# Kernel tuning notes

Measured on AMD Instinct MI355X. Metric: run time of the kernel, lower is better.

The kernel has to match this reference:

```python
import math
import jax, jax.numpy as jnp
import numpy as np

B, S, M, D, H, FF = 2, 2048, 64, 1024, 16, 4096
HD = D // H


def setup_inputs() -> dict:
    key = jax.random.key(0)
    ks = jax.random.split(key, 16)
    w = lambda k, shape: jax.random.normal(k, shape, dtype=jnp.float32) * 0.02
    # RoPE angles: theta_i = pos / 10000^(2i/head_dim)
    inv_freq = 1.0 / (10000.0 ** (jnp.arange(0, HD, 2, dtype=jnp.float32) / HD))
    ang = jnp.arange(S, dtype=jnp.float32)[:, None] * inv_freq[None, :]  # (S, HD//2)
    return {
        "tgt": jax.random.normal(ks[0], (B, S, D), dtype=jnp.float32),
        "memory": jax.random.normal(ks[1], (B, M, D), dtype=jnp.float32),
        "rope_cos": jnp.cos(ang),
        "rope_sin": jnp.sin(ang),
        "W_qkv": w(ks[2], (D, 3 * D)), "b_qkv": jnp.zeros((3 * D,), jnp.float32),
        "W_o": w(ks[3], (D, D)), "b_o": jnp.zeros((D,), jnp.float32),
        "Wq_c": w(ks[4], (D, D)), "bq_c": jnp.zeros((D,), jnp.float32),
        "Wk_c": w(ks[5], (D, D)), "bk_c": jnp.zeros((D,), jnp.float32),
        "Wv_c": w(ks[6], (D, D)), "bv_c": jnp.zeros((D,), jnp.float32),
        "W_co": w(ks[7], (D, D)), "b_co": jnp.zeros((D,), jnp.float32),
        "W1": w(ks[8], (D, FF)), "b1": jnp.zeros((FF,), jnp.float32),
        "W2": w(ks[9], (FF, D)), "b2": jnp.zeros((D,), jnp.float32),
        "g1": jnp.ones((D,), jnp.float32), "be1": jnp.zeros((D,), jnp.float32),
        "g2": jnp.ones((D,), jnp.float32), "be2": jnp.zeros((D,), jnp.float32),
        "g3": jnp.ones((D,), jnp.float32), "be3": jnp.zeros((D,), jnp.float32),
    }


def _layer_norm(x, g, b, eps=1e-5):
    mu = jnp.mean(x, axis=-1, keepdims=True)
    var = jnp.mean(jnp.square(x - mu), axis=-1, keepdims=True)
    return (x - mu) * jax.lax.rsqrt(var + eps) * g + b


def _apply_rope(x, cos, sin):
    # x: (B, H, S, HD); cos/sin: (S, HD//2). Pairs (even, odd) rotated as complex.
    xe, xo = x[..., 0::2], x[..., 1::2]
    c = cos[None, None]
    s = sin[None, None]
    re = xe * c - xo * s
    im = xe * s + xo * c
    return jnp.stack([re, im], axis=-1).reshape(x.shape)


def reference(tgt, memory, rope_cos, rope_sin, W_qkv, b_qkv, W_o, b_o,
              Wq_c, bq_c, Wk_c, bk_c, Wv_c, bv_c, W_co, b_co,
              W1, b1, W2, b2, g1, be1, g2, be2, g3, be3):
    b, s, d = tgt.shape
    scale = 1.0 / math.sqrt(HD)

    # --- RoPE self-attention (causal) ---
    x = _layer_norm(tgt, g1, be1)
    qkv = (x @ W_qkv + b_qkv).reshape(b, s, 3, H, HD)
    qkv = jnp.transpose(qkv, (2, 0, 3, 1, 4))  # (3, b, H, s, HD)
    q, k, v = qkv[0], qkv[1], qkv[2]
    q = _apply_rope(q, rope_cos[:s], rope_sin[:s])
    k = _apply_rope(k, rope_cos[:s], rope_sin[:s])
    attn = jnp.einsum('bhqd,bhkd->bhqk', q, k) * scale
    causal = jnp.tril(jnp.ones((s, s), dtype=bool))
    attn = jnp.where(causal[None, None], attn, -1e9)
    attn = jax.nn.softmax(attn, axis=-1)
    sa = jnp.einsum('bhqk,bhkd->bhqd', attn, v)
    sa = jnp.transpose(sa, (0, 2, 1, 3)).reshape(b, s, d)
    tgt = tgt + (sa @ W_o + b_o)

    # --- cross-attention to memory (no positional encoding) ---
    x = _layer_norm(tgt, g2, be2)
    m = memory.shape[1]
    qc = (x @ Wq_c + bq_c).reshape(b, s, H, HD).transpose(0, 2, 1, 3)
    kc = (memory @ Wk_c + bk_c).reshape(b, m, H, HD).transpose(0, 2, 1, 3)
    vc = (memory @ Wv_c + bv_c).reshape(b, m, H, HD).transpose(0, 2, 1, 3)
    ca = jax.nn.softmax(jnp.einsum('bhqd,bhkd->bhqk', qc, kc) * scale, axis=-1)
    co = jnp.einsum('bhqk,bhkd->bhqd', ca, vc)
    co = jnp.transpose(co, (0, 2, 1, 3)).reshape(b, s, d)
    tgt = tgt + (co @ W_co + b_co)

    # --- FFN (exact GELU, dropout disabled = eval) ---
    x = _layer_norm(tgt, g3, be3)
    ffn = jax.nn.gelu(x @ W1 + b1, approximate=False) @ W2 + b2
    return tgt + ffn
```

## Files before the change

kernel.cpp:

```cpp
#include <hip/hip_runtime.h>

typedef unsigned short u16;
typedef short bf16x8 __attribute__((ext_vector_type(8)));
typedef float f32x4 __attribute__((ext_vector_type(4)));

#define HN 16
#define SD 64
#define SEQ 2048
#define DM 1024
#define QSC 0.18033688f

__device__ __forceinline__ float bf2f(u16 h) {
  return __uint_as_float(((unsigned int)h) << 16);
}
__device__ __forceinline__ u16 f2bf(float f) {
  unsigned int x = __float_as_uint(f);
  x += 0x7fffu + ((x >> 16) & 1u);
  return (u16)(x >> 16);
}
__device__ __forceinline__ float geluf(float x) {
  return 0.5f * x * (1.0f + erff(x * 0.70710678118654752f));
}
__device__ __forceinline__ void load_lds16(const u16* g, u16* l) {
  __builtin_amdgcn_global_load_lds(
      (const __attribute__((address_space(1))) void*)g,
      (__attribute__((address_space(3))) void*)l, 16, 0, 0);
}

__device__ __forceinline__ void trans_tile(const float* __restrict__ in,
                                           u16* __restrict__ out, int K, int N,
                                           int tx, int ty, int tid,
                                           u16 (*T)[72]) {
  const int n0 = tx * 64, k0 = ty * 64;
#pragma unroll
  for (int it = 0; it < 2; ++it) {
    const int t = it * 256 + tid, r = t >> 3, c = (t & 7) * 8;
    const float* src = &in[(size_t)(k0 + r) * N + n0 + c];
    float4 d0 = *(const float4*)src;
    float4 d1 = *(const float4*)(src + 4);
    T[r][c + 0] = f2bf(d0.x);
    T[r][c + 1] = f2bf(d0.y);
    T[r][c + 2] = f2bf(d0.z);
    T[r][c + 3] = f2bf(d0.w);
    T[r][c + 4] = f2bf(d1.x);
    T[r][c + 5] = f2bf(d1.y);
    T[r][c + 6] = f2bf(d1.z);
    T[r][c + 7] = f2bf(d1.w);
  }
  __syncthreads();
#pragma unroll
  for (int it = 0; it < 2; ++it) {
    const int t = it * 256 + tid, r = t >> 3, c = (t & 7) * 8;
    uint4 d;
    u16* p = (u16*)&d;
#pragma unroll
    for (int j = 0; j < 8; ++j) p[j] = T[c + j][r];
    *(uint4*)&out[(size_t)(n0 + r) * K + k0 + c] = d;
  }
}

__global__ __launch_bounds__(256) void prep1(
    const float* __restrict__ Wqkv, const float* __restrict__ Wo,
    const float* __restrict__ Wqc, const float* __restrict__ Wkc,
    const float* __restrict__ Wvc, const float* __restrict__ Wco,
    u16* __restrict__ Tqkv, u16* __restrict__ To, u16* __restrict__ Tqc,
    u16* __restrict__ Tkc, u16* __restrict__ Tvc, u16* __restrict__ Tco,
    const float* __restrict__ mem, u16* __restrict__ memb) {
  __shared__ u16 T[64][72];
  const int t = blockIdx.x, tid = threadIdx.x;
  if (t < 768) {
    trans_tile(Wqkv, Tqkv, 1024, 3072, t % 48, t / 48, tid, T);
    return;
  }
  if (t < 2048) {
    const int u = t - 768, m = u >> 8, sub = u & 255;
    const float* in;
    u16* out;
    if (m == 0) { in = Wo; out = To; }
    else if (m == 1) { in = Wqc; out = Tqc; }
    else if (m == 2) { in = Wkc; out = Tkc; }
    else if (m == 3) { in = Wvc; out = Tvc; }
    else { in = Wco; out = Tco; }
    trans_tile(in, out, 1024, 1024, sub & 15, sub >> 4, tid, T);
    return;
  }
  const int i = ((t - 2048) * 256 + tid) * 4;
  float4 d = *(const float4*)&mem[i];
  uint2 o;
  u16* po = (u16*)&o;
  po[0] = f2bf(d.x);
  po[1] = f2bf(d.y);
  po[2] = f2bf(d.z);
  po[3] = f2bf(d.w);
  *(uint2*)&memb[i] = o;
}

__global__ __launch_bounds__(256) void prep2(const float* __restrict__ W1,
                                             const float* __restrict__ W2,
                                             u16* __restrict__ T1,
                                             u16* __restrict__ T2) {
  __shared__ u16 T[64][72];
  const int t = blockIdx.x, tid = threadIdx.x;
  if (t < 1024) {
    trans_tile(W1, T1, 1024, 4096, t & 63, t >> 6, tid, T);
  } else {
    const int u = t - 1024;
    trans_tile(W2, T2, 4096, 1024, u & 15, u >> 4, tid, T);
  }
}

__global__ __launch_bounds__(256) void ln_kernel(
    const float* __restrict__ x, const float* __restrict__ g,
    const float* __restrict__ be, u16* __restrict__ y) {
  const int row = blockIdx.x, tid = threadIdx.x;
  const float* xr = x + (size_t)row * DM;
  float4 d = *(const float4*)&xr[tid * 4];
  float v[4] = {d.x, d.y, d.z, d.w};
  float s1 = 0.f, s2 = 0.f;
#pragma unroll
  for (int j = 0; j < 4; ++j) {
    s1 += v[j];
    s2 += v[j] * v[j];
  }
#pragma unroll
  for (int dd = 1; dd < 64; dd <<= 1) {
    s1 += __shfl_xor(s1, dd, 64);
    s2 += __shfl_xor(s2, dd, 64);
  }
  __shared__ float p1[4], p2[4];
  const int lane = tid & 63, wv = tid >> 6;
  if (lane == 0) {
    p1[wv] = s1;
    p2[wv] = s2;
  }
  __syncthreads();
  s1 = p1[0] + p1[1] + p1[2] + p1[3];
  s2 = p2[0] + p2[1] + p2[2] + p2[3];
  const float mu = s1 * (1.f / DM);
  const float rs = rsqrtf(fmaxf(s2 * (1.f / DM) - mu * mu, 0.f) + 1e-5f);
  float4 gg = *(const float4*)&g[tid * 4];
  float4 bb = *(const float4*)&be[tid * 4];
  const float gv[4] = {gg.x, gg.y, gg.z, gg.w};
  const float bv[4] = {bb.x, bb.y, bb.z, bb.w};
  uint2 o;
  u16* po = (u16*)&o;
#pragma unroll
  for (int j = 0; j < 4; ++j) po[j] = f2bf((v[j] - mu) * rs * gv[j] + bv[j]);
  *(uint2*)&y[(size_t)row * DM + tid * 4] = o;
}

template <int EPI, int TM>
__global__ __launch_bounds__(256) void gemm_bt(
    const u16* __restrict__ A, const u16* __restrict__ Bt,
    const float* __restrict__ bias, const float* __restrict__ resid,
    void* __restrict__ C0, u16* __restrict__ C1, u16* __restrict__ C2, int M,
    int N, int K, int rpbl, float sc, const float* __restrict__ rcos,
    const float* __restrict__ rsin) {
  constexpr int MI = TM / 32;
  __shared__ __align__(16) u16 As[TM][64];
  __shared__ __align__(16) u16 Bs[128][64];
  const int tid = threadIdx.x;
  const int lane = tid & 63, wv = tid >> 6;
  const int l16 = lane & 15, quad = lane >> 4;

  if (EPI == 6 && blockIdx.z) {
    Bt = (const u16*)C1;
    bias = resid;
  }

  int bx = blockIdx.x, by = blockIdx.y;
  const int gx = gridDim.x, gy = gridDim.y;
  if ((gy & 7) == 0) {
    const int f = by * gx + bx;
    const int c = f & 7, j = f >> 3;
    const int jm = j / gx;
    by = c * (gy >> 3) + jm;
    bx = j - jm * gx;
  }
  const int m0 = by * TM, n0 = bx * 128;
  const int wm = (wv >> 1) * (TM / 2), wn = (wv & 1) * 64;

  const int srow = lane >> 3;
  const int sblk = (lane & 7) ^ srow;
  const u16* ag[MI];
  const u16* bg[4];
  u16* la[MI];
  u16* lb[4];
#pragma unroll
  for (int i = 0; i < MI; ++i) {
    const int r0 = i * 32 + wv * 8;
    ag[i] = A + (size_t)(m0 + r0 + srow) * K + sblk * 8;
    la[i] = &As[r0][0] + lane * 8;
  }
#pragma unroll
  for (int i = 0; i < 4; ++i) {
    const int r0 = i * 32 + wv * 8;
    bg[i] = Bt + (size_t)(n0 + r0 + srow) * K + sblk * 8;
    lb[i] = &Bs[r0][0] + lane * 8;
  }

  f32x4 acc[MI][4] = {};

  for (int k0 = 0; k0 < K; k0 += 64) {
    __syncthreads();
#pragma unroll
    for (int i = 0; i < MI; ++i) load_lds16(ag[i] + k0, la[i]);
#pragma unroll
    for (int i = 0; i < 4; ++i) load_lds16(bg[i] + k0, lb[i]);
    __syncthreads();
#pragma unroll
    for (int kk = 0; kk < 2; ++kk) {
      bf16x8 af[MI], bfr[4];
#pragma unroll
      for (int mi = 0; mi < MI; ++mi) {
        const int row = wm + mi * 16 + l16;
        const int blk = (kk * 4 + quad) ^ (row & 7);
        af[mi] = *(const bf16x8*)&As[row][blk * 8];
      }
#pragma unroll
      for (int ni = 0; ni < 4; ++ni) {
        const int row = wn + ni * 16 + l16;
        const int blk = (kk * 4 + quad) ^ (row & 7);
        bfr[ni] = *(const bf16x8*)&Bs[row][blk * 8];
      }
#pragma unroll
      for (int mi = 0; mi < MI; ++mi)
#pragma unroll
        for (int ni = 0; ni < 4; ++ni)
          acc[mi][ni] = __builtin_amdgcn_mfma_f32_16x16x32_bf16(
              af[mi], bfr[ni], acc[mi][ni], 0, 0, 0);
    }
  }

  const int SL = 1 << rpbl;
#pragma unroll
  for (int mi = 0; mi < MI; ++mi) {
#pragma unroll
    for (int ni = 0; ni < 4; ++ni) {
#pragma unroll
      for (int r = 0; r < 4; ++r) {
        const int row = m0 + wm + mi * 16 + quad * 4 + r;
        const int col = n0 + wn + ni * 16 + l16;
        float vv = acc[mi][ni][r] + bias[col];
        if (EPI == 1) {
          vv += resid[(size_t)row * N + col];
          ((float*)C0)[(size_t)row * N + col] = vv;
        } else if (EPI == 2) {
          ((u16*)C0)[(size_t)row * N + col] = f2bf(geluf(vv));
        } else if (EPI == 3) {
          const float partner = __shfl_xor(vv, 1);
          const int which = col >> 10;
          const int nn = col & 1023;
          const int h = nn >> 6, hd = nn & 63;
          const int b = row >> rpbl;
          const int s = row & (SL - 1);
          if (which == 2) {
            C2[(((size_t)b * HN + h) * SD + hd) * SL + s] = f2bf(vv);
          } else {
            const int p = hd >> 1;
            const float cv = rcos[s * 32 + p];
            const float sv2 = rsin[s * 32 + p];
            float o = (hd & 1) ? (partner * sv2 + vv * cv)
                               : (vv * cv - partner * sv2);
            if (which == 0) o *= QSC;
            u16* dst = (which == 0) ? (u16*)C0 : C1;
            dst[(((size_t)b * HN + h) * SL + s) * SD + hd] = f2bf(o);
          }
        } else if (EPI == 4) {
          vv *= sc;
          const int h = col >> 6, hd = col & 63;
          const int b = row >> rpbl;
          const int s = row & (SL - 1);
          ((u16*)C0)[(((size_t)b * HN + h) * SL + s) * SD + hd] = f2bf(vv);
        } else if (EPI == 5) {
          const int h = col >> 6, hd = col & 63;
          const int b = row >> rpbl;
          const int s = row & (SL - 1);
          ((u16*)C0)[(((size_t)b * HN + h) * SD + hd) * SL + s] = f2bf(vv);
        } else if (EPI == 6) {
          const int h = col >> 6, hd = col & 63;
          const int b = row >> rpbl;
          const int s = row & (SL - 1);
          if (blockIdx.z == 0)
            ((u16*)C0)[(((size_t)b * HN + h) * SL + s) * SD + hd] = f2bf(vv);
          else
            C2[(((size_t)b * HN + h) * SD + hd) * SL + s] = f2bf(vv);
        } else {
          ((u16*)C0)[(size_t)row * N + col] = f2bf(vv);
        }
      }
    }
  }
}

template <int EPI>
__global__ __launch_bounds__(512, 2) void gemm8p(
    const u16* __restrict__ A, const u16* __restrict__ Bt,
    const float* __restrict__ bias, void* __restrict__ C0,
    u16* __restrict__ C1, u16* __restrict__ C2, int M, int N, int K, int rpbl,
    const float* __restrict__ rcos, const float* __restrict__ rsin) {
  __shared__ __align__(16) u16 L[4][2][8192];
  const int tid = threadIdx.x;
  const int lane = tid & 63, wv = tid >> 6;
  const int l16 = lane & 15, quad = lane >> 4;
  const int bx = blockIdx.x, by = blockIdx.y;
  const int m0 = by * 256, n0 = bx * 256;
  const int wm = (wv >> 2) * 128, wn = (wv & 3) * 64;
  const int nk = K >> 6;

  const u16* Ag = A + (size_t)m0 * K;
  const u16* Bg = Bt + (size_t)n0 * K;

  auto stage = [&](int mat, int h, int st) {
    const int tt = st < nk ? st : nk - 1;
    const int k0 = tt << 6;
    u16* dst = &L[mat * 2 + h][st & 1][0];
    const u16* src = mat ? Bg : Ag;
#pragma unroll
    for (int j = 0; j < 2; ++j) {
      const int li = wv * 2 + j;
      const int p = li * 8 + (lane >> 3);
      const int b = lane & 7;
      const int g = b ^ (p & 7);
      const int row = 2 * p + (g >> 2);
      load_lds16(src + (size_t)row * K + k0 + h * 32 + (g & 3) * 8,
                 dst + li * 512 + lane * 8);
    }
  };

  f32x4 acc[8][4] = {};
  bf16x8 bfr[4];

#define PHASE(CB, KK, MH, RB, SM, SH, ST, VM)                                \
  {                                                                          \
    const u16* Ar = &L[KK][CB][0];                                           \
    const u16* Br = &L[2 + KK][CB][0];                                       \
    bf16x8 af[4];                                                            \
    _Pragma("unroll") for (int mi = 0; mi < 4; ++mi) {                       \
      const int R = wm + MH * 64 + mi * 16 + l16;                            \
      const int p = R >> 1, g = (R & 1) * 4 + quad, b = g ^ (p & 7);         \
      af[mi] = *(const bf16x8*)&Ar[p * 64 + b * 8];                          \
    }                                                                        \
    if (RB) {                                                                \
      _Pragma("unroll") for (int ni = 0; ni < 4; ++ni) {                     \
        const int R = wn + ni * 16 + l16;                                    \
        const int p = R >> 1, g = (R & 1) * 4 + quad, b = g ^ (p & 7);       \
        bfr[ni] = *(const bf16x8*)&Br[p * 64 + b * 8];                       \
      }                                                                      \
    }                                                                        \
    stage(SM, SH, ST);                                                       \
    __builtin_amdgcn_s_barrier();                                            \
    asm volatile("s_waitcnt lgkmcnt(0)" ::: "memory");                       \
    __builtin_amdgcn_s_setprio(1);                                           \
    _Pragma("unroll") for (int mi = 0; mi < 4; ++mi)                         \
        _Pragma("unroll") for (int ni = 0; ni < 4; ++ni) acc[MH * 4 + mi]    \
            [ni] = __builtin_amdgcn_mfma_f32_16x16x32_bf16(                  \
                af[mi], bfr[ni], acc[MH * 4 + mi][ni], 0, 0, 0);             \
    __builtin_amdgcn_s_setprio(0);                                           \
    if (VM) asm volatile("s_waitcnt vmcnt(8)" ::: "memory");                 \
    __builtin_amdgcn_s_barrier();                                            \
  }

  stage(0, 0, 0);
  stage(1, 0, 0);
  stage(0, 1, 0);
  stage(1, 1, 0);
  stage(0, 0, 1);
  stage(1, 0, 1);
  asm volatile("s_waitcnt vmcnt(8)" ::: "memory");
  __builtin_amdgcn_s_barrier();

  for (int t = 0; t < nk; ++t) {
    const int cb = t & 1;
    PHASE(cb, 0, 0, true, 0, 1, t + 1, false)
    PHASE(cb, 0, 1, false, 1, 1, t + 1, true)
    PHASE(cb, 1, 0, true, 0, 0, t + 2, false)
    PHASE(cb, 1, 1, false, 1, 0, t + 2, true)
  }
#undef PHASE

  const int SL = 1 << rpbl;
#pragma unroll
  for (int mi = 0; mi < 8; ++mi) {
#pragma unroll
    for (int ni = 0; ni < 4; ++ni) {
#pragma unroll
      for (int r = 0; r < 4; ++r) {
        const int row = m0 + wm + mi * 16 + quad * 4 + r;
        const int col = n0 + wn + ni * 16 + l16;
        float vv = acc[mi][ni][r] + bias[col];
        if (EPI == 2) {
          ((u16*)C0)[(size_t)row * N + col] = f2bf(geluf(vv));
        } else if (EPI == 3) {
          const float partner = __shfl_xor(vv, 1);
          const int which = col >> 10;
          const int nn = col & 1023;
          const int h = nn >> 6, hd = nn & 63;
          const int b = row >> rpbl;
          const int s = row & (SL - 1);
          if (which == 2) {
            C2[(((size_t)b * HN + h) * SD + hd) * SL + s] = f2bf(vv);
          } else {
            const int p = hd >> 1;
            const float cv = rcos[s * 32 + p];
            const float sv2 = rsin[s * 32 + p];
            float o = (hd & 1) ? (partner * sv2 + vv * cv)
                               : (vv * cv - partner * sv2);
            if (which == 0) o *= QSC;
            u16* dst = (which == 0) ? (u16*)C0 : C1;
            dst[(((size_t)b * HN + h) * SL + s) * SD + hd] = f2bf(o);
          }
        } else {
          ((u16*)C0)[(size_t)row * N + col] = f2bf(vv);
        }
      }
    }
  }
}

template <int CAUSAL>
__global__ __launch_bounds__(512, 4) void attn_kernel(
    const u16* __restrict__ q, const u16* __restrict__ k,
    const u16* __restrict__ vt, u16* __restrict__ out, int kv_len) {
  __shared__ u16 Qs[128][72], Ks[64][72], VTs[64][72];
  __shared__ u16 Ps[128][68];
  const int tid = threadIdx.x;
  const int lane = tid & 63, wv = tid >> 6;
  const int t2 = wv >> 2, w4 = wv & 3;
  const int l16 = lane & 15, quad = lane >> 4;
  const int bx = blockIdx.x, bh = blockIdx.y;
  const int qtA = bx;
  const int qtB = CAUSAL ? (31 - bx) : (bx + 16);
  const int qt = t2 ? qtB : qtA;
  const u16* qb = q + (size_t)bh * SEQ * SD;
  const u16* kb = k + (size_t)bh * kv_len * SD;
  const u16* vtb = vt + (size_t)bh * SD * kv_len;

#pragma unroll
  for (int it = 0; it < 2; ++it) {
    const int t = it * 512 + tid, r = t >> 3, c = (t & 7) * 8;
    const int qrow = (r < 64) ? (qtA * 64 + r) : (qtB * 64 + (r - 64));
    *(uint4*)&Qs[r][c] = *(const uint4*)&qb[(size_t)qrow * SD + c];
  }

  f32x4 o_acc[4] = {};
  float l_i[4] = {};

  const int ktiles = CAUSAL ? (qtB + 1) : ((kv_len + 63) >> 6);
  const int sr = tid >> 3, sc8 = (tid & 7) * 8;

  for (int kt = 0; kt < ktiles; ++kt) {
    const uint4 kd = *(const uint4*)&kb[((size_t)kt * 64 + sr) * SD + sc8];
    const uint4 vd = *(const uint4*)&vtb[(size_t)sr * kv_len + kt * 64 + sc8];
    __syncthreads();
    *(uint4*)&Ks[sr][sc8] = kd;
    *(uint4*)&VTs[sr][sc8] = vd;
    __syncthreads();

    if (kt <= qt) {
      const int roff = t2 * 64 + w4 * 16;
      f32x4 s_acc[4] = {};
#pragma unroll
      for (int kk = 0; kk < 64; kk += 32) {
        const bf16x8 aq = *(const bf16x8*)&Qs[roff + l16][kk + quad * 8];
#pragma unroll
        for (int ni = 0; ni < 4; ++ni) {
          const bf16x8 bk = *(const bf16x8*)&Ks[ni * 16 + l16][kk + quad * 8];
          s_acc[ni] = __builtin_amdgcn_mfma_f32_16x16x32_bf16(aq, bk, s_acc[ni],
                                                              0, 0, 0);
        }
      }
      float rsum[4] = {0.f, 0.f, 0.f, 0.f};
      const bool dg = CAUSAL && (kt == qt);
#pragma unroll
      for (int ni = 0; ni < 4; ++ni)
#pragma unroll
        for (int r = 0; r < 4; ++r) {
          float sv = s_acc[ni][r];
          if (dg && (ni * 16 + l16 > w4 * 16 + quad * 4 + r)) sv = -1e9f;
          const float pe = __builtin_amdgcn_exp2f(sv);
          rsum[r] += pe;
          Ps[wv * 16 + quad * 4 + r][ni * 16 + l16] =
              (u16)(__float_as_uint(pe) >> 16);
        }
#pragma unroll
      for (int r = 0; r < 4; ++r) {
#pragma unroll
        for (int dd = 1; dd < 16; dd <<= 1)
          rsum[r] += __shfl_xor(rsum[r], dd, 64);
        l_i[r] += rsum[r];
      }
#pragma unroll
      for (int kk = 0; kk < 64; kk += 32) {
        const bf16x8 ap = *(const bf16x8*)&Ps[wv * 16 + l16][kk + quad * 8];
#pragma unroll
        for (int ni = 0; ni < 4; ++ni) {
          const bf16x8 bv = *(const bf16x8*)&VTs[ni * 16 + l16][kk + quad * 8];
          o_acc[ni] = __builtin_amdgcn_mfma_f32_16x16x32_bf16(ap, bv, o_acc[ni],
                                                              0, 0, 0);
        }
      }
    }
  }

  const int b = bh >> 4, h = bh & 15;
#pragma unroll
  for (int r = 0; r < 4; ++r) {
    const float inv = 1.f / l_i[r];
    const int s = qt * 64 + w4 * 16 + quad * 4 + r;
#pragma unroll
    for (int ni = 0; ni < 4; ++ni)
      out[((size_t)b * SEQ + s) * DM + h * SD + ni * 16 + l16] =
          f2bf(o_acc[ni][r] * inv);
  }
}

extern "C" void kernel_launch(void* const* d_in, const int* in_sizes, int n_in,
                              void* d_out, int out_size, void* d_ws,
                              size_t ws_size, hipStream_t stream) {
  (void)in_sizes;
  (void)n_in;
  (void)out_size;
  (void)ws_size;
  const float* tgt = (const float*)d_in[0];
  const float* mem = (const float*)d_in[1];
  const float* rc = (const float*)d_in[2];
  const float* rsn = (const float*)d_in[3];
  const float* W_qkv = (const float*)d_in[4];
  const float* b_qkv = (const float*)d_in[5];
  const float* W_o = (const float*)d_in[6];
  const float* b_o = (const float*)d_in[7];
  const float* Wq_c = (const float*)d_in[8];
  const float* bq_c = (const float*)d_in[9];
  const float* Wk_c = (const float*)d_in[10];
  const float* bk_c = (const float*)d_in[11];
  const float* Wv_c = (const float*)d_in[12];
  const float* bv_c = (const float*)d_in[13];
  const float* W_co = (const float*)d_in[14];
  const float* b_co = (const float*)d_in[15];
  const float* W1 = (const float*)d_in[16];
  const float* b1 = (const float*)d_in[17];
  const float* W2 = (const float*)d_in[18];
  const float* b2 = (const float*)d_in[19];
  const float* g1 = (const float*)d_in[20];
  const float* be1 = (const float*)d_in[21];
  const float* g2 = (const float*)d_in[22];
  const float* be2 = (const float*)d_in[23];
  const float* g3 = (const float*)d_in[24];
  const float* be3 = (const float*)d_in[25];

  const size_t M1 = 1048576;
  u16* w = (u16*)d_ws;
  u16* WTqkv = w;
  u16* WTo = w + 3 * M1;
  u16* WTqc = w + 4 * M1;
  u16* WTkc = w + 5 * M1;
  u16* WTvc = w + 6 * M1;
  u16* WTco = w + 7 * M1;
  u16* WT1 = w;
  u16* WT2 = w + 4 * M1;
  u16* xb = w + 8 * M1;
  u16* qb = w + 12 * M1;
  u16* kb = w + 16 * M1;
  u16* vbT = w + 20 * M1;
  u16* at = w + 24 * M1;
  u16* kc = w + 28 * M1;
  u16* vcT = kc + 131072;
  u16* memb = vcT + 131072;
  u16* ffh = qb;
  float* res = (float*)d_out;

  dim3 blk(256), blk512(512);
  prep1<<<2176, blk, 0, stream>>>(W_qkv, W_o, Wq_c, Wk_c, Wv_c, W_co, WTqkv,
                                  WTo, WTqc, WTkc, WTvc, WTco, mem, memb);

  ln_kernel<<<4096, blk, 0, stream>>>(tgt, g1, be1, xb);
  gemm8p<3><<<dim3(12, 16), blk512, 0, stream>>>(xb, WTqkv, b_qkv, qb, kb, vbT,
                                                 4096, 3072, 1024, 11, rc, rsn);
  attn_kernel<1><<<dim3(16, 32), blk512, 0, stream>>>(qb, kb, vbT, at, 2048);
  gemm_bt<1, 64><<<dim3(8, 64), blk, 0, stream>>>(at, WTo, b_o, tgt, res,
                                                  nullptr, nullptr, 4096, 1024,
                                                  1024, 0, 1.f, nullptr,
                                                  nullptr);
  ln_kernel<<<4096, blk, 0, stream>>>(res, g2, be2, xb);
  gemm_bt<4, 64><<<dim3(8, 64), blk, 0, stream>>>(
      xb, WTqc, bq_c, nullptr, qb, nullptr, nullptr, 4096, 1024, 1024, 11, QSC,
      nullptr, nullptr);
  gemm_bt<6, 64><<<dim3(8, 2, 2), blk, 0, stream>>>(
      memb, WTkc, bk_c, bv_c, kc, WTvc, vcT, 128, 1024, 1024, 6, 1.f, nullptr,
      nullptr);
  attn_kernel<0><<<dim3(16, 32), blk512, 0, stream>>>(qb, kc, vcT, at, 64);
  gemm_bt<1, 64><<<dim3(8, 64), blk, 0, stream>>>(at, WTco, b_co, res, res,
                                                  nullptr, nullptr, 4096, 1024,
                                                  1024, 0, 1.f, nullptr,
                                                  nullptr);
  prep2<<<2048, blk, 0, stream>>>(W1, W2, WT1, WT2);
  ln_kernel<<<4096, blk, 0, stream>>>(res, g3, be3, xb);
  gemm8p<2><<<dim3(16, 16), blk512, 0, stream>>>(xb, WT1, b1, ffh, nullptr,
                                                 nullptr, 4096, 4096, 1024, 0,
                                                 nullptr, nullptr);
  gemm_bt<1, 64><<<dim3(8, 64), blk, 0, stream>>>(ffh, WT2, b2, res, res,
                                                  nullptr, nullptr, 4096, 1024,
                                                  4096, 0, 1.f, nullptr,
                                                  nullptr);
}
```

Measured before the change: 490.3 us.

## Precompute LDS addresses, unroll k-loop by two, and remap workgroups across XCDs

```diff
diff --git a/kernel.cpp b/kernel.cpp
--- a/kernel.cpp
+++ b/kernel.cpp
@@ -25,6 +25,10 @@
   __builtin_amdgcn_global_load_lds(
       (const __attribute__((address_space(1))) void*)g,
       (__attribute__((address_space(3))) void*)l, 16, 0, 0);
+}
+__device__ __forceinline__ unsigned ldsoff(const u16* p) {
+  return (unsigned)(unsigned long long)(
+      const __attribute__((address_space(3))) u16*)p;
 }
 
 __device__ __forceinline__ void trans_tile(const float* __restrict__ in,
@@ -303,7 +307,18 @@
   const int tid = threadIdx.x;
   const int lane = tid & 63, wv = tid >> 6;
   const int l16 = lane & 15, quad = lane >> 4;
-  const int bx = blockIdx.x, by = blockIdx.y;
+  int bx = blockIdx.x, by = blockIdx.y;
+  {
+    const int gx = gridDim.x;
+    const int nwg = gx * gridDim.y;
+    if ((nwg & 7) == 0) {
+      const int f = by * gx + bx;
+      const int q = nwg >> 3;
+      const int wg = (f & 7) * q + (f >> 3);
+      by = wg / gx;
+      bx = wg - by * gx;
+    }
+  }
   const int m0 = by * 256, n0 = bx * 256;
   const int wm = (wv >> 2) * 128, wn = (wv & 3) * 64;
   const int nk = K >> 6;
@@ -328,37 +343,53 @@
     }
   };
 
+  unsigned aaddr[2][4], baddr[4];
+  {
+    const unsigned Lb = ldsoff(&L[0][0][0]);
+#pragma unroll
+    for (int MH = 0; MH < 2; ++MH)
+#pragma unroll
+      for (int mi = 0; mi < 4; ++mi) {
+        const int R = wm + MH * 64 + mi * 16 + l16;
+        const int p = R >> 1, g = (R & 1) * 4 + quad, b = g ^ (p & 7);
+        aaddr[MH][mi] = Lb + (unsigned)(p * 64 + b * 8) * 2u;
+      }
+#pragma unroll
+    for (int ni = 0; ni < 4; ++ni) {
+      const int R = wn + ni * 16 + l16;
+      const int p = R >> 1, g = (R & 1) * 4 + quad, b = g ^ (p & 7);
+      baddr[ni] = Lb + 65536u + (unsigned)(p * 64 + b * 8) * 2u;
+    }
+  }
+
   f32x4 acc[8][4] = {};
   bf16x8 bfr[4];
 
-#define PHASE(CB, KK, MH, RB, SM, SH, ST, VM)                                \
-  {                                                                          \
-    const u16* Ar = &L[KK][CB][0];                                           \
-    const u16* Br = &L[2 + KK][CB][0];                                       \
-    bf16x8 af[4];                                                            \
-    _Pragma("unroll") for (int mi = 0; mi < 4; ++mi) {                       \
-      const int R = wm + MH * 64 + mi * 16 + l16;                            \
-      const int p = R >> 1, g = (R & 1) * 4 + quad, b = g ^ (p & 7);         \
-      af[mi] = *(const bf16x8*)&Ar[p * 64 + b * 8];                          \
-    }                                                                        \
-    if (RB) {                                                                \
-      _Pragma("unroll") for (int ni = 0; ni < 4; ++ni) {                     \
-        const int R = wn + ni * 16 + l16;                                    \
-        const int p = R >> 1, g = (R & 1) * 4 + quad, b = g ^ (p & 7);       \
-        bfr[ni] = *(const bf16x8*)&Br[p * 64 + b * 8];                       \
-      }                                                                      \
-    }                                                                        \
-    stage(SM, SH, ST);                                                       \
-    __builtin_amdgcn_s_barrier();                                            \
-    asm volatile("s_waitcnt lgkmcnt(0)" ::: "memory");                       \
-    __builtin_amdgcn_s_setprio(1);                                           \
-    _Pragma("unroll") for (int mi = 0; mi < 4; ++mi)                         \
-        _Pragma("unroll") for (int ni = 0; ni < 4; ++ni) acc[MH * 4 + mi]    \
-            [ni] = __builtin_amdgcn_mfma_f32_16x16x32_bf16(                  \
-                af[mi], bfr[ni], acc[MH * 4 + mi][ni], 0, 0, 0);             \
-    __builtin_amdgcn_s_setprio(0);                                           \
-    if (VM) asm volatile("s_waitcnt vmcnt(8)" ::: "memory");                 \
-    __builtin_amdgcn_s_barrier();                                            \
+#define PHASE(CB, KK, MH, RB, SM, SH, ST, VM)                                 \
+  {                                                                           \
+    bf16x8 af[4];                                                             \
+    _Pragma("unroll") for (int mi = 0; mi < 4; ++mi)                          \
+        asm volatile("ds_read_b128 %0, %1 offset:%2"                          \
+                     : "=v"(af[mi])                                           \
+                     : "v"(aaddr[MH][mi]), "i"((KK)*32768 + (CB)*16384));     \
+    if (RB) {                                                                 \
+      _Pragma("unroll") for (int ni = 0; ni < 4; ++ni)                        \
+          asm volatile("ds_read_b128 %0, %1 offset:%2"                        \
+                       : "=v"(bfr[ni])                                        \
+                       : "v"(baddr[ni]), "i"((KK)*32768 + (CB)*16384));       \
+    }                                                                         \
+    stage(SM, SH, ST);                                                        \
+    __builtin_amdgcn_s_barrier();                                             \
+    asm volatile("s_waitcnt lgkmcnt(0)");                                     \
+    __builtin_amdgcn_sched_barrier(0);                                        \
+    __builtin_amdgcn_s_setprio(1);                                            \
+    _Pragma("unroll") for (int mi = 0; mi < 4; ++mi)                          \
+        _Pragma("unroll") for (int ni = 0; ni < 4; ++ni) acc[(MH)*4 + mi]     \
+            [ni] = __builtin_amdgcn_mfma_f32_16x16x32_bf16(                   \
+                af[mi], bfr[ni], acc[(MH)*4 + mi][ni], 0, 0, 0);              \
+    __builtin_amdgcn_s_setprio(0);                                            \
+    if (VM) asm volatile("s_waitcnt vmcnt(8)");                               \
+    __builtin_amdgcn_s_barrier();                                             \
   }
 
   stage(0, 0, 0);
@@ -367,15 +398,18 @@
   stage(1, 1, 0);
   stage(0, 0, 1);
   stage(1, 0, 1);
-  asm volatile("s_waitcnt vmcnt(8)" ::: "memory");
+  asm volatile("s_waitcnt vmcnt(8)");
   __builtin_amdgcn_s_barrier();
 
-  for (int t = 0; t < nk; ++t) {
-    const int cb = t & 1;
-    PHASE(cb, 0, 0, true, 0, 1, t + 1, false)
-    PHASE(cb, 0, 1, false, 1, 1, t + 1, true)
-    PHASE(cb, 1, 0, true, 0, 0, t + 2, false)
-    PHASE(cb, 1, 1, false, 1, 0, t + 2, true)
+  for (int t = 0; t < nk; t += 2) {
+    PHASE(0, 0, 0, true, 0, 1, t + 1, false)
+    PHASE(0, 0, 1, false, 1, 1, t + 1, true)
+    PHASE(0, 1, 0, true, 0, 0, t + 2, false)
+    PHASE(0, 1, 1, false, 1, 0, t + 2, true)
+    PHASE(1, 0, 0, true, 0, 1, t + 2, false)
+    PHASE(1, 0, 1, false, 1, 1, t + 2, true)
+    PHASE(1, 1, 0, true, 0, 0, t + 3, false)
+    PHASE(1, 1, 1, false, 1, 0, t + 3, true)
   }
 #undef PHASE
 
```

New measurement: 491.5 us. About the same (+0.3%).
